# Kernel optimization log

Hardware: AMD Instinct MI355X
Metric: run time of the kernel (lower is better)

## Reference

```python
import jax, jax.numpy as jnp
import numpy as np

B = 128          # batch (requests)
SPEC = 4         # drafts per request (uniform here, code handles ragged)
V = 128000       # vocab size
MAX_SPEC_LEN = SPEC
NT = B * SPEC    # total flattened draft tokens
PLACEHOLDER = -1


def setup_inputs() -> dict:
    key = jax.random.key(0)
    k1, k2, k3, k4, k5 = jax.random.split(key, 5)
    draft_token_ids = jax.random.randint(k1, (NT,), 0, V, dtype=jnp.int32)
    draft_probs = jax.nn.softmax(2.0 * jax.random.normal(k2, (NT, V), dtype=jnp.float32), axis=-1)
    target_probs = jax.nn.softmax(2.0 * jax.random.normal(k3, (NT, V), dtype=jnp.float32), axis=-1)
    uniform_probs = jax.random.uniform(k4, (NT,), dtype=jnp.float32)
    bonus_token_ids = jax.random.randint(k5, (B,), 0, V, dtype=jnp.int32)
    cu_num_draft_tokens = (jnp.arange(1, B + 1) * SPEC).astype(jnp.int32)
    return {
        "draft_probs": draft_probs,
        "target_probs": target_probs,
        "uniform_probs": uniform_probs,
        "draft_token_ids": draft_token_ids,
        "cu_num_draft_tokens": cu_num_draft_tokens,
        "bonus_token_ids": bonus_token_ids,
    }


def reference(draft_probs, target_probs, uniform_probs, draft_token_ids,
              cu_num_draft_tokens, bonus_token_ids):
    # Faithful vectorized version of rejection_random_sample_kernel.
    nt = target_probs.shape[0]
    L = MAX_SPEC_LEN
    cu = cu_num_draft_tokens.astype(jnp.int32)
    prev = jnp.concatenate([jnp.zeros((1,), cu.dtype), cu[:-1]])   # start_idx per req
    ndraft = cu - prev                                              # [B]
    pos = jnp.arange(L, dtype=jnp.int32)                            # [L]
    tok_idx = prev[:, None] + pos[None, :]                          # [B,L] global token idx
    valid = pos[None, :] < ndraft[:, None]                          # [B,L]
    safe_idx = jnp.clip(tok_idx, 0, nt - 1)

    d_ids = draft_token_ids[safe_idx]                               # [B,L]
    tp = target_probs[safe_idx, d_ids]                              # target prob of draft token
    dp = draft_probs[safe_idx, d_ids]                               # draft prob of draft token
    uu = uniform_probs[safe_idx]

    # neutral values outside valid range: ratio=1, uniform=1 keep carries unchanged
    ratio = jnp.where(valid & (dp > 0), tp / jnp.where(dp > 0, dp, 1.0), 1.0)
    uu = jnp.where(valid, uu, 1.0)
    dpos = valid & (dp > 0)

    def step(carry, xs):
        pi, U = carry                       # [B] each
        r, u, ok = xs
        pi = jnp.minimum(pi * r, 1.0)
        U = U * u
        accept = ok & (pi >= U)
        return (pi, U), accept

    init = (jnp.ones((cu.shape[0],), jnp.float32), jnp.ones((cu.shape[0],), jnp.float32))
    _, accept = jax.lax.scan(step, init, (ratio.T, uu.T, dpos.T))   # accept: [L,B]
    accept = accept.T                                                # [B,L]

    # last accepted position (or -1); 'rejected' == final-iteration accept failed
    last = jnp.max(jnp.where(accept, pos[None, :], -1), axis=1)      # [B]
    rejected = (ndraft > 0) & (last != ndraft - 1)

    # copy accepted draft tokens [0..last]
    out_L = jnp.where(pos[None, :] <= last[:, None], d_ids, PLACEHOLDER).astype(jnp.int32)
    out = jnp.concatenate([out_L, jnp.full((cu.shape[0], 1), PLACEHOLDER, jnp.int32)], axis=1)

    # recovered token: argmax of target_probs row at position last+1
    rec_row = jnp.clip(prev + last + 1, 0, nt - 1)
    rec_id = jnp.argmax(target_probs[rec_row], axis=-1).astype(jnp.int32)   # [B]

    write_col = jnp.where(rejected, last + 1, ndraft)
    write_val = jnp.where(rejected, rec_id, bonus_token_ids.astype(jnp.int32))
    out = out.at[jnp.arange(cu.shape[0]), write_col].set(write_val)
    return out
```

## Files before the change

kernel.cpp:

```cpp
#include <hip/hip_runtime.h>
#include <hip/hip_bf16.h>
#include <float.h>

#define SPLITS 16


__global__ void chain_kernel(
    const float* __restrict__ draft_probs,
    const float* __restrict__ target_probs,
    const float* __restrict__ uniform_probs,
    const int*   __restrict__ draft_ids,
    const int*   __restrict__ cu,
    const int*   __restrict__ bonus,
    int*         __restrict__ out,
    unsigned long long* __restrict__ packed,
    int* __restrict__ flag, int* __restrict__ recrow, int* __restrict__ writecol,
    int B, int V, int NT, int L)
{
    const int b = blockIdx.x * blockDim.x + threadIdx.x;
    if (b >= B) return;

    const int start = (b == 0) ? 0 : cu[b - 1];
    const int nd    = cu[b] - start;
    const int nchain = (nd < L) ? nd : L;

    float pi = 1.0f, U = 1.0f;
    int last = -1;
    int* row = out + (size_t)b * (L + 1);

    for (int i = 0; i < nchain; ++i) {
        const int t   = start + i;
        const int did = draft_ids[t];
        row[i] = did;
        const size_t off = (size_t)t * (size_t)V + (size_t)did;
        const float tp = target_probs[off];
        const float dp = draft_probs[off];
        const float uu = uniform_probs[t];
        const bool ok = dp > 0.0f;
        const float r = ok ? (tp / dp) : 1.0f;
        pi = fminf(pi * r, 1.0f);
        U  = U * uu;
        if (ok && pi >= U) last = i;
    }
    for (int i = last + 1; i <= L; ++i) row[i] = -1;

    const bool rejected = (nd > 0) && (last != nd - 1);
    if (!rejected) {
        row[nd] = bonus[b];
    }
    int rr = start + last + 1;
    rr = rr < 0 ? 0 : (rr > NT - 1 ? NT - 1 : rr);

    flag[b]     = rejected ? 1 : 0;
    recrow[b]   = rr;
    writecol[b] = last + 1;
    packed[b]   = 0ull;
}

__global__ __launch_bounds__(256) void argmax_partial_kernel(
    const float* __restrict__ target_probs,
    const unsigned long long* __restrict__ ,
    unsigned long long* __restrict__ packed,
    const int* __restrict__ flag, const int* __restrict__ recrow,
    int V)
{
    const int b = blockIdx.x;
    const int s = blockIdx.y;
    if (!flag[b]) return;

    const int tid = threadIdx.x;
    const float* rowbase = target_probs + (size_t)recrow[b] * (size_t)V;
    const int n4 = V >> 2;
    const int chunk4 = (n4 + SPLITS - 1) / SPLITS;
    const int lo4 = s * chunk4;
    const int hi4 = (lo4 + chunk4 < n4) ? lo4 + chunk4 : n4;

    float bestv = -FLT_MAX;
    int   besti = 0x7fffffff;
    const float4* rowp = (const float4*)rowbase;
    for (int j = lo4 + tid; j < hi4; j += 256) {
        const float4 v = rowp[j];
        const int base = j << 2;
        if (v.x > bestv) { bestv = v.x; besti = base;     }
        if (v.y > bestv) { bestv = v.y; besti = base + 1; }
        if (v.z > bestv) { bestv = v.z; besti = base + 2; }
        if (v.w > bestv) { bestv = v.w; besti = base + 3; }
    }
    if (s == SPLITS - 1) {
        for (int j = (n4 << 2) + tid; j < V; j += 256) {
            const float v = rowbase[j];
            if (v > bestv) { bestv = v; besti = j; }
        }
    }

    __shared__ float sv[256];
    __shared__ int   si[256];
    sv[tid] = bestv;
    si[tid] = besti;
    __syncthreads();
    for (int w = 128; w > 0; w >>= 1) {
        if (tid < w) {
            const float ov = sv[tid + w];
            const int   oi = si[tid + w];
            if (ov > sv[tid] || (ov == sv[tid] && oi < si[tid])) {
                sv[tid] = ov;
                si[tid] = oi;
            }
        }
        __syncthreads();
    }
    if (tid == 0 && sv[0] > -FLT_MAX) {
        const unsigned int fbits = __float_as_uint(sv[0]);
        const unsigned long long p =
            ((unsigned long long)fbits << 32) |
            (unsigned long long)(0xFFFFFFFFu - (unsigned int)si[0]);
        atomicMax(&packed[b], p);
    }
}

__global__ void finalize_kernel(
    int* __restrict__ out,
    const unsigned long long* __restrict__ packed,
    const int* __restrict__ flag, const int* __restrict__ writecol,
    int B, int L)
{
    const int b = blockIdx.x * blockDim.x + threadIdx.x;
    if (b >= B) return;
    if (!flag[b]) return;
    const unsigned long long p = packed[b];
    const int idx = (int)(0xFFFFFFFFu - (unsigned int)(p & 0xFFFFFFFFull));
    out[(size_t)b * (L + 1) + writecol[b]] = idx;
}

extern "C" void kernel_launch(void* const* d_in, const int* in_sizes, int n_in,
                              void* d_out, int out_size, void* d_ws, size_t ws_size,
                              hipStream_t stream) {
    const float* draft_probs   = (const float*)d_in[0];
    const float* target_probs  = (const float*)d_in[1];
    const float* uniform_probs = (const float*)d_in[2];
    const int*   draft_ids     = (const int*)d_in[3];
    const int*   cu            = (const int*)d_in[4];
    const int*   bonus         = (const int*)d_in[5];
    int*         out           = (int*)d_out;

    const int NT = in_sizes[2];
    const int V  = in_sizes[0] / NT;
    const int B  = in_sizes[4];
    const int L  = out_size / B - 1;

    unsigned long long* packed = (unsigned long long*)d_ws;
    int* flag     = (int*)((char*)d_ws + (size_t)B * 8);
    int* recrow   = (int*)((char*)d_ws + (size_t)B * 8 + (size_t)B * 4);
    int* writecol = (int*)((char*)d_ws + (size_t)B * 8 + (size_t)B * 8);

    const int bthreads = 256;
    const int bblocks  = (B + bthreads - 1) / bthreads;

    chain_kernel<<<bblocks, bthreads, 0, stream>>>(
        draft_probs, target_probs, uniform_probs, draft_ids, cu, bonus,
        out, packed, flag, recrow, writecol, B, V, NT, L);

    dim3 grid(B, SPLITS);
    argmax_partial_kernel<<<grid, 256, 0, stream>>>(
        target_probs, nullptr, packed, flag, recrow, V);

    finalize_kernel<<<bblocks, bthreads, 0, stream>>>(
        out, packed, flag, writecol, B, L);
}
```

Before: 409.3 us.

## Fuse chain, argmax and finalize kernels into one launch with last-block completion

Merges the three kernels into one grid of B×SPLITS blocks. Every block recomputes the short acceptance chain with its loads unrolled. Split blocks then reduce the argmax and use an atomic counter so the last-finishing block writes the recovered token. A memset replaces the per-request reset of the workspace. This removes two extra launches and the dependency round-trips between them, at the cost of redundant chain work in every block and an extra memset.

```diff
diff --git a/kernel.cpp b/kernel.cpp
--- a/kernel.cpp
+++ b/kernel.cpp
@@ -1,11 +1,11 @@
 #include <hip/hip_runtime.h>
-#include <hip/hip_bf16.h>
 #include <float.h>
 
 #define SPLITS 16
+#define CHAIN_UNROLL 8
 
 
-__global__ void chain_kernel(
+__global__ __launch_bounds__(256) void fused_kernel(
     const float* __restrict__ draft_probs,
     const float* __restrict__ target_probs,
     const float* __restrict__ uniform_probs,
@@ -14,66 +14,82 @@
     const int*   __restrict__ bonus,
     int*         __restrict__ out,
     unsigned long long* __restrict__ packed,
-    int* __restrict__ flag, int* __restrict__ recrow, int* __restrict__ writecol,
+    unsigned int* __restrict__ count,
     int B, int V, int NT, int L)
 {
-    const int b = blockIdx.x * blockDim.x + threadIdx.x;
-    if (b >= B) return;
+    const int b   = blockIdx.x;
+    const int s   = blockIdx.y;
+    const int tid = threadIdx.x;
 
-    const int start = (b == 0) ? 0 : cu[b - 1];
-    const int nd    = cu[b] - start;
+    const int start  = (b == 0) ? 0 : cu[b - 1];
+    const int nd     = cu[b] - start;
     const int nchain = (nd < L) ? nd : L;
+    const int nc8    = (nchain < CHAIN_UNROLL) ? nchain : CHAIN_UNROLL;
 
     float pi = 1.0f, U = 1.0f;
     int last = -1;
-    int* row = out + (size_t)b * (L + 1);
+    int mydid = -1;
 
-    for (int i = 0; i < nchain; ++i) {
-        const int t   = start + i;
-        const int did = draft_ids[t];
-        row[i] = did;
-        const size_t off = (size_t)t * (size_t)V + (size_t)did;
-        const float tp = target_probs[off];
-        const float dp = draft_probs[off];
-        const float uu = uniform_probs[t];
-        const bool ok = dp > 0.0f;
-        const float r = ok ? (tp / dp) : 1.0f;
+    int   did[CHAIN_UNROLL];
+    float tp[CHAIN_UNROLL], dp[CHAIN_UNROLL], uu[CHAIN_UNROLL];
+
+#pragma unroll
+    for (int i = 0; i < CHAIN_UNROLL; ++i) {
+        did[i] = (i < nc8) ? draft_ids[start + i]     : -1;
+        uu[i]  = (i < nc8) ? uniform_probs[start + i] : 1.0f;
+    }
+#pragma unroll
+    for (int i = 0; i < CHAIN_UNROLL; ++i) {
+        if (i < nc8) {
+            const size_t off = (size_t)(start + i) * (size_t)V + (size_t)did[i];
+            tp[i] = target_probs[off];
+            dp[i] = draft_probs[off];
+        } else { tp[i] = 0.0f; dp[i] = 0.0f; }
+    }
+#pragma unroll
+    for (int i = 0; i < CHAIN_UNROLL; ++i) {
+        if (i < nc8) {
+            const bool  ok = dp[i] > 0.0f;
+            const float r  = ok ? (tp[i] / dp[i]) : 1.0f;
+            pi = fminf(pi * r, 1.0f);
+            U  = U * uu[i];
+            if (ok && pi >= U) last = i;
+            if (tid == i) mydid = did[i];
+        }
+    }
+    for (int i = CHAIN_UNROLL; i < nchain; ++i) {
+        const int t = start + i;
+        const int d = draft_ids[t];
+        const size_t off = (size_t)t * (size_t)V + (size_t)d;
+        const float tpv = target_probs[off];
+        const float dpv = draft_probs[off];
+        const bool  ok  = dpv > 0.0f;
+        const float r   = ok ? (tpv / dpv) : 1.0f;
         pi = fminf(pi * r, 1.0f);
-        U  = U * uu;
+        U *= uniform_probs[t];
         if (ok && pi >= U) last = i;
+        if (tid == i) mydid = d;
     }
-    for (int i = last + 1; i <= L; ++i) row[i] = -1;
 
     const bool rejected = (nd > 0) && (last != nd - 1);
-    if (!rejected) {
-        row[nd] = bonus[b];
+
+    if (s == 0 && tid <= L) {
+        int val = (tid <= last) ? mydid : -1;
+        if (!rejected && tid == nd) val = bonus[b];
+        if (!(rejected && tid == last + 1))
+            out[(size_t)b * (L + 1) + tid] = val;
     }
+
+    if (!rejected) return;
+
     int rr = start + last + 1;
     rr = rr < 0 ? 0 : (rr > NT - 1 ? NT - 1 : rr);
+    const float* rowbase = target_probs + (size_t)rr * (size_t)V;
 
-    flag[b]     = rejected ? 1 : 0;
-    recrow[b]   = rr;
-    writecol[b] = last + 1;
-    packed[b]   = 0ull;
-}
-
-__global__ __launch_bounds__(256) void argmax_partial_kernel(
-    const float* __restrict__ target_probs,
-    const unsigned long long* __restrict__ ,
-    unsigned long long* __restrict__ packed,
-    const int* __restrict__ flag, const int* __restrict__ recrow,
-    int V)
-{
-    const int b = blockIdx.x;
-    const int s = blockIdx.y;
-    if (!flag[b]) return;
-
-    const int tid = threadIdx.x;
-    const float* rowbase = target_probs + (size_t)recrow[b] * (size_t)V;
-    const int n4 = V >> 2;
+    const int n4     = V >> 2;
     const int chunk4 = (n4 + SPLITS - 1) / SPLITS;
-    const int lo4 = s * chunk4;
-    const int hi4 = (lo4 + chunk4 < n4) ? lo4 + chunk4 : n4;
+    const int lo4    = s * chunk4;
+    const int hi4    = (lo4 + chunk4 < n4) ? lo4 + chunk4 : n4;
 
     float bestv = -FLT_MAX;
     int   besti = 0x7fffffff;
@@ -109,27 +125,23 @@
         }
         __syncthreads();
     }
-    if (tid == 0 && sv[0] > -FLT_MAX) {
-        const unsigned int fbits = __float_as_uint(sv[0]);
-        const unsigned long long p =
-            ((unsigned long long)fbits << 32) |
-            (unsigned long long)(0xFFFFFFFFu - (unsigned int)si[0]);
-        atomicMax(&packed[b], p);
+
+    if (tid == 0) {
+        if (sv[0] > -FLT_MAX) {
+            const unsigned int fbits = __float_as_uint(sv[0]);
+            const unsigned long long p =
+                ((unsigned long long)fbits << 32) |
+                (unsigned long long)(0xFFFFFFFFu - (unsigned int)si[0]);
+            atomicMax(&packed[b], p);
+        }
+        __threadfence();
+        const unsigned int old = atomicAdd(&count[b], 1u);
+        if (old == SPLITS - 1) {
+            const unsigned long long p = atomicMax(&packed[b], 0ull);
+            const int idx = (int)(0xFFFFFFFFu - (unsigned int)(p & 0xFFFFFFFFull));
+            out[(size_t)b * (L + 1) + (last + 1)] = idx;
+        }
     }
-}
-
-__global__ void finalize_kernel(
-    int* __restrict__ out,
-    const unsigned long long* __restrict__ packed,
-    const int* __restrict__ flag, const int* __restrict__ writecol,
-    int B, int L)
-{
-    const int b = blockIdx.x * blockDim.x + threadIdx.x;
-    if (b >= B) return;
-    if (!flag[b]) return;
-    const unsigned long long p = packed[b];
-    const int idx = (int)(0xFFFFFFFFu - (unsigned int)(p & 0xFFFFFFFFull));
-    out[(size_t)b * (L + 1) + writecol[b]] = idx;
 }
 
 extern "C" void kernel_launch(void* const* d_in, const int* in_sizes, int n_in,
@@ -149,21 +161,12 @@
     const int L  = out_size / B - 1;
 
     unsigned long long* packed = (unsigned long long*)d_ws;
-    int* flag     = (int*)((char*)d_ws + (size_t)B * 8);
-    int* recrow   = (int*)((char*)d_ws + (size_t)B * 8 + (size_t)B * 4);
-    int* writecol = (int*)((char*)d_ws + (size_t)B * 8 + (size_t)B * 8);
+    unsigned int* count = (unsigned int*)((char*)d_ws + (size_t)B * 8);
 
-    const int bthreads = 256;
-    const int bblocks  = (B + bthreads - 1) / bthreads;
-
-    chain_kernel<<<bblocks, bthreads, 0, stream>>>(
-        draft_probs, target_probs, uniform_probs, draft_ids, cu, bonus,
-        out, packed, flag, recrow, writecol, B, V, NT, L);
+    hipMemsetAsync(d_ws, 0, (size_t)B * 12, stream);
 
     dim3 grid(B, SPLITS);
-    argmax_partial_kernel<<<grid, 256, 0, stream>>>(
-        target_probs, nullptr, packed, flag, recrow, V);
-
-    finalize_kernel<<<bblocks, bthreads, 0, stream>>>(
-        out, packed, flag, writecol, B, L);
+    fused_kernel<<<grid, 256, 0, stream>>>(
+        draft_probs, target_probs, uniform_probs, draft_ids, cu, bonus,
+        out, packed, count, B, V, NT, L);
 }
```

Result: slower. 434.5 us (+6.1%).
